# Optimization experiments

Measured on AMD Instinct MI355X. Metric: run time of the kernel, lower is better.

Reference implementation:

```python
import jax, jax.numpy as jnp
import numpy as np

B, S, D, H, F = 64, 256, 512, 8, 2048
NB = 2
L = NB + 2 * NB  # blocks_1 (NB) + blocks_2 (2*NB) = 6 attention layers
DH = D // H
FC1, FC2 = 512, 256  # final_fc_dim, final_fc_dim // 2


def setup_inputs() -> dict:
    key = jax.random.key(0)
    ks = jax.random.split(key, 32)
    w = lambda k, shape, s: jax.random.normal(k, shape, dtype=jnp.float32) * s
    sD = D ** -0.5
    return {
        "q_embed_data": w(ks[0], (B, S, D), 1.0),
        "qa_embed_data": w(ks[1], (B, S, D), 1.0),
        "Wq": w(ks[2], (L, D, D), sD), "bq": jnp.zeros((L, D), jnp.float32),
        "Wk": w(ks[3], (L, D, D), sD), "bk": jnp.zeros((L, D), jnp.float32),
        "Wv": w(ks[4], (L, D, D), sD), "bv": jnp.zeros((L, D), jnp.float32),
        "Wo": w(ks[5], (L, D, D), sD), "bo": jnp.zeros((L, D), jnp.float32),
        "gammas": w(ks[6], (L, H), 1.0),
        "ln1_g": jnp.ones((L, D), jnp.float32), "ln1_b": jnp.zeros((L, D), jnp.float32),
        "W1": w(ks[7], (L, D, F), sD), "b1": jnp.zeros((L, F), jnp.float32),
        "W2": w(ks[8], (L, F, D), F ** -0.5), "b2": jnp.zeros((L, D), jnp.float32),
        "ln2_g": jnp.ones((L, D), jnp.float32), "ln2_b": jnp.zeros((L, D), jnp.float32),
        "O1": w(ks[9], (2 * D, FC1), (2 * D) ** -0.5), "bO1": jnp.zeros((FC1,), jnp.float32),
        "O2": w(ks[10], (FC1, FC2), FC1 ** -0.5), "bO2": jnp.zeros((FC2,), jnp.float32),
        "O3": w(ks[11], (FC2, 1), FC2 ** -0.5), "bO3": jnp.zeros((1,), jnp.float32),
    }


def _layer_norm(x, g, b):
    mu = x.mean(-1, keepdims=True)
    var = ((x - mu) ** 2).mean(-1, keepdims=True)
    return (x - mu) * jax.lax.rsqrt(var + 1e-5) * g + b


def _akt_attention(q, k, v, mask, gamma, zero_pad):
    # q,k,v: [B,H,S,DH]; mask: [S,S] bool; gamma: [H]
    neg = jnp.float32(-1e32)
    scores = jnp.einsum('bhqd,bhkd->bhqk', q, k) / np.sqrt(DH).astype(np.float32)
    # monotonic distance-decay (detached in the original): softmax'd scores -> cumulative distance
    sm = jax.nn.softmax(jnp.where(mask, scores, neg), axis=-1) * mask
    sm = jax.lax.stop_gradient(sm)
    distcum = jnp.cumsum(sm, axis=-1)
    disttot = jnp.sum(sm, axis=-1, keepdims=True)
    idx = jnp.arange(S)
    pos = jnp.abs(idx[:, None] - idx[None, :]).astype(jnp.float32)  # |x1 - x2|
    dist = jnp.sqrt(jnp.clip((disttot - distcum) * pos, 0.0, None))
    g = -jax.nn.softplus(gamma)[None, :, None, None]
    total_effect = jnp.clip(jnp.exp(dist * g), 1e-5, 1e5)
    scores = jnp.where(mask, scores * total_effect, neg)
    attn = jax.nn.softmax(scores, axis=-1)
    if zero_pad:
        attn = attn.at[:, :, 0, :].set(0.0)  # zero first query row
    out = jnp.einsum('bhqk,bhkd->bhqd', attn, v)
    return out, attn


def reference(q_embed_data, qa_embed_data, Wq, bq, Wk, bk, Wv, bv, Wo, bo, gammas,
              ln1_g, ln1_b, W1, b1, W2, b2, ln2_g, ln2_b, O1, bO1, O2, bO2, O3, bO3):
    idx = jnp.arange(S)
    mask_incl = idx[:, None] >= idx[None, :]  # mask==1: current + past
    mask_excl = idx[:, None] > idx[None, :]   # mask==0: strictly past

    def block(i, query, key_, vals, incl, zero_pad, apply_pos):
        proj = lambda x, W, b: (x @ W + b).reshape(B, S, H, DH).transpose(0, 2, 1, 3)
        qh, kh, vh = proj(query, Wq[i], bq[i]), proj(key_, Wk[i], bk[i]), proj(vals, Wv[i], bv[i])
        o, attn = _akt_attention(qh, kh, vh, mask_incl if incl else mask_excl, gammas[i], zero_pad)
        o = o.transpose(0, 2, 1, 3).reshape(B, S, D) @ Wo[i] + bo[i]
        q2 = _layer_norm(query + o, ln1_g[i], ln1_b[i])
        if apply_pos:
            h = jax.nn.relu(q2 @ W1[i] + b1[i]) @ W2[i] + b2[i]
            q2 = _layer_norm(q2 + h, ln2_g[i], ln2_b[i])
        return q2, attn

    y = qa_embed_data
    x = q_embed_data
    li = 0
    for _ in range(NB):  # blocks_1: knowledge encoder, self-attn, mask=1
        y, _ = block(li, y, y, y, incl=True, zero_pad=False, apply_pos=True)
        li += 1
    attn = None
    flag_first = True
    for _ in range(2 * NB):  # blocks_2: alternating question self-attn / knowledge retriever
        if flag_first:
            x, _ = block(li, x, x, x, incl=True, zero_pad=False, apply_pos=False)
            flag_first = False
        else:
            x, attn = block(li, x, x, y, incl=False, zero_pad=True, apply_pos=True)
            flag_first = True
        li += 1

    concat_q = jnp.concatenate([x, q_embed_data], axis=-1)  # [B,S,2D]
    h = jax.nn.relu(concat_q @ O1 + bO1)
    h = jax.nn.relu(h @ O2 + bO2)
    preds = jax.nn.sigmoid((h @ O3 + bO3)[..., 0])  # [B,S]
    return preds
```

## Files before the change

kernel.cpp:

```cpp
#include <hip/hip_runtime.h>

typedef unsigned short u16;
typedef unsigned int u32;
typedef short short8 __attribute__((ext_vector_type(8)));
typedef float f32x4 __attribute__((ext_vector_type(4)));

#define DEV static __device__ __forceinline__

DEV u16 f2bf(float f) {
  u32 u = __builtin_bit_cast(u32, f);
  u32 r = u + 0x7FFFu + ((u >> 16) & 1u);
  return (u16)(r >> 16);
}
DEV float bf2f(u16 h) { u32 u = ((u32)h) << 16; return __builtin_bit_cast(float, u); }

DEV u32 cvtpk(float lo, float hi_) {
  u32 r;
  asm("v_cvt_pk_bf16_f32 %0, %1, %2" : "=v"(r) : "v"(lo), "v"(hi_));
  return r;
}

DEV void async16(const u16* g, u16* l) {
  __builtin_amdgcn_global_load_lds((const __attribute__((address_space(1))) void*)g,
                                   (__attribute__((address_space(3))) void*)l, 16, 0, 0);
}

template<bool RELU, bool OUTBF, bool RESID, bool SPLIT3>
__global__ __launch_bounds__(256, 2) void gemm_kernel(
    const u16* __restrict__ A, const u16* __restrict__ A2, int KA,
    int lda, int lda2,
    const u16* __restrict__ Bt, int K,
    const float* __restrict__ bias, const float* __restrict__ resid,
    float* __restrict__ Cf, u16* __restrict__ Cb, u16* __restrict__ Cb2, u16* __restrict__ Cb3,
    int ldc)
{
  __shared__ u16 smem[2][16384];
  const int tid = threadIdx.x, wave = tid >> 6, lane = tid & 63;
  const int m0 = blockIdx.x * 128, n0 = blockIdx.y * 128;
  const int wr = wave >> 1, wc = wave & 1;
  const int lj = lane & 15, hi = lane >> 4;

  f32x4 acc[4][4];
  const f32x4 zz = {0.f, 0.f, 0.f, 0.f};
#pragma unroll
  for (int i = 0; i < 4; i++)
#pragma unroll
    for (int j = 0; j < 4; j++) acc[i][j] = zz;

  const int nkt = K / 64;

  auto stage = [&](int buf, int kt) {
    int kofs = kt * 64;
    const u16* sa; int la;
    if (kofs < KA) { sa = A + kofs; la = lda; }
    else           { sa = A2 + (kofs - KA); la = lda2; }
#pragma unroll
    for (int i = 0; i < 8; i++) {
      int c = wave * 8 + i;
      if (c < 16) {
        const u16* g = sa + (size_t)(m0 + c * 8 + (lane >> 3)) * la + (lane & 7) * 8;
        async16(g, &smem[buf][c * 512]);
      } else {
        const u16* g = Bt + (size_t)(n0 + (c - 16) * 8 + (lane >> 3)) * K + kofs + (lane & 7) * 8;
        async16(g, &smem[buf][c * 512]);
      }
    }
  };

  stage(0, 0);
  int cur = 0;
  for (int kt = 0; kt < nkt; kt++) {
    __syncthreads();
    if (kt + 1 < nkt) stage(cur ^ 1, kt + 1);
    const u16* la_ = &smem[cur][0];
    const u16* lb_ = &smem[cur][8192];
#pragma unroll
    for (int ks = 0; ks < 2; ks++) {
      short8 af[4], bfr[4];
#pragma unroll
      for (int mi = 0; mi < 4; mi++)
        af[mi] = *(const short8*)(la_ + (wr * 64 + mi * 16 + lj) * 64 + ks * 32 + hi * 8);
#pragma unroll
      for (int ni = 0; ni < 4; ni++)
        bfr[ni] = *(const short8*)(lb_ + (wc * 64 + ni * 16 + lj) * 64 + ks * 32 + hi * 8);
#pragma unroll
      for (int mi = 0; mi < 4; mi++)
#pragma unroll
        for (int ni = 0; ni < 4; ni++)
          acc[mi][ni] = __builtin_amdgcn_mfma_f32_16x16x32_bf16(af[mi], bfr[ni], acc[mi][ni], 0, 0, 0);
    }
    cur ^= 1;
  }

  u16* outB = Cb;
  int nloc = n0;
  if (SPLIT3) {
    int sec = n0 >> 9;
    outB = (sec == 0) ? Cb : (sec == 1) ? Cb2 : Cb3;
    nloc = n0 & 511;
  }

  float bv[4];
#pragma unroll
  for (int ni = 0; ni < 4; ni++) bv[ni] = bias[n0 + wc * 64 + ni * 16 + lj];
#pragma unroll
  for (int mi = 0; mi < 4; mi++)
#pragma unroll
    for (int r = 0; r < 4; r++) {
      int row = m0 + wr * 64 + mi * 16 + hi * 4 + r;
      size_t rb = (size_t)row * ldc;
#pragma unroll
      for (int ni = 0; ni < 4; ni++) {
        int col = nloc + wc * 64 + ni * 16 + lj;
        float v = acc[mi][ni][r] + bv[ni];
        if (RESID) v += resid[rb + col];
        if (RELU) v = fmaxf(v, 0.f);
        if (OUTBF) outB[rb + col] = f2bf(v);
        else Cf[rb + col] = v;
      }
    }
}

template<bool RELU, bool SPLIT3>
__global__ __launch_bounds__(512) void gemm256_kernel(
    const u16* __restrict__ A, int lda,
    const u16* __restrict__ Bt, int K,
    const float* __restrict__ bias,
    u16* __restrict__ Cb, u16* __restrict__ Cb2, u16* __restrict__ Cb3, int ldc)
{
  __shared__ u16 smem[65536];
  const int tid = threadIdx.x, wave = tid >> 6, lane = tid & 63;
  const int m0 = blockIdx.x * 256, n0 = blockIdx.y * 256;
  const int wm = wave >> 2, wn = wave & 3;
  const int lj = lane & 15, hi = lane >> 4;
  const int srow = wave * 8 + (lane >> 3);
  const int schunk = (lane & 7) ^ ((lane >> 3) & 7);

  f32x4 acc[8][4];
  const f32x4 zz = {0.f, 0.f, 0.f, 0.f};
#pragma unroll
  for (int i = 0; i < 8; i++)
#pragma unroll
    for (int j = 0; j < 4; j++) acc[i][j] = zz;

  const int nkt = K / 64;

  auto stageA = [&](int buf, int kt, int seg) {
    const u16* g = A + (size_t)(m0 + seg * 64 + srow) * lda + kt * 64 + schunk * 8;
    async16(g, &smem[buf * 16384 + (seg * 64 + wave * 8) * 64]);
  };
  auto stageB = [&](int buf, int kt, int seg) {
    const u16* g = Bt + (size_t)(n0 + seg * 64 + srow) * K + kt * 64 + schunk * 8;
    async16(g, &smem[32768 + buf * 16384 + (seg * 64 + wave * 8) * 64]);
  };

#pragma unroll
  for (int seg = 0; seg < 4; seg++) stageA(0, 0, seg);
#pragma unroll
  for (int seg = 0; seg < 4; seg++) stageB(0, 0, seg);

  int cur = 0;
  for (int t = 0; t < nkt; t++) {
    const bool pf = (t + 1 < nkt);
    const char* aB = (const char*)smem + cur * 32768;
    const char* bB = (const char*)smem + 65536 + cur * 32768;
#pragma unroll
    for (int ph = 0; ph < 4; ph++) {
      const int mh = ph >> 1, nh = ph & 1;
      if (pf) {
        if (ph < 2) { stageA(cur ^ 1, t + 1, ph * 2); stageA(cur ^ 1, t + 1, ph * 2 + 1); }
        else        { stageB(cur ^ 1, t + 1, (ph - 2) * 2); stageB(cur ^ 1, t + 1, (ph - 2) * 2 + 1); }
      }
      if (ph == 0) {
        if (pf) asm volatile("s_waitcnt vmcnt(2)" ::: "memory");
        else    asm volatile("s_waitcnt vmcnt(0)" ::: "memory");
      }
      __builtin_amdgcn_s_barrier();

      short8 af[4][2], bfr[2][2];
#pragma unroll
      for (int mi = 0; mi < 4; mi++) {
        int row = wm * 128 + (mh * 4 + mi) * 16 + lj;
#pragma unroll
        for (int ks = 0; ks < 2; ks++)
          af[mi][ks] = *(const short8*)(aB + row * 128 + ((ks * 64 + hi * 16) ^ ((row & 7) << 4)));
      }
#pragma unroll
      for (int ni = 0; ni < 2; ni++) {
        int row = wn * 64 + (nh * 2 + ni) * 16 + lj;
#pragma unroll
        for (int ks = 0; ks < 2; ks++)
          bfr[ni][ks] = *(const short8*)(bB + row * 128 + ((ks * 64 + hi * 16) ^ ((row & 7) << 4)));
      }
      __builtin_amdgcn_s_setprio(1);
#pragma unroll
      for (int mi = 0; mi < 4; mi++)
#pragma unroll
        for (int ni = 0; ni < 2; ni++)
#pragma unroll
          for (int ks = 0; ks < 2; ks++)
            acc[mh * 4 + mi][nh * 2 + ni] =
                __builtin_amdgcn_mfma_f32_16x16x32_bf16(af[mi][ks], bfr[ni][ks],
                                                        acc[mh * 4 + mi][nh * 2 + ni], 0, 0, 0);
      __builtin_amdgcn_s_setprio(0);
      __builtin_amdgcn_s_barrier();
    }
    cur ^= 1;
  }

  u16* outB = Cb;
  int nloc = n0;
  if (SPLIT3) {
    int sec = n0 >> 9;
    outB = (sec == 0) ? Cb : (sec == 1) ? Cb2 : Cb3;
    nloc = n0 & 511;
  }

  float bv[4];
#pragma unroll
  for (int ni = 0; ni < 4; ni++) bv[ni] = bias[n0 + wn * 64 + ni * 16 + lj];
#pragma unroll
  for (int mi = 0; mi < 8; mi++)
#pragma unroll
    for (int r = 0; r < 4; r++) {
      int row = m0 + wm * 128 + mi * 16 + hi * 4 + r;
      size_t rb = (size_t)row * ldc;
#pragma unroll
      for (int ni = 0; ni < 4; ni++) {
        int col = nloc + wn * 64 + ni * 16 + lj;
        float v = acc[mi][ni][r] + bv[ni];
        if (RELU) v = fmaxf(v, 0.f);
        outB[rb + col] = f2bf(v);
      }
    }
}

__global__ __launch_bounds__(512) void gemmln_kernel(
    const u16* __restrict__ A, int lda,
    const u16* __restrict__ Bt, int K,
    const float* __restrict__ bias, const float* __restrict__ resid,
    const float* __restrict__ gamma, const float* __restrict__ beta,
    float* __restrict__ outF, u16* __restrict__ outB)
{
  __shared__ u16 smem[73728];
  const int tid = threadIdx.x, wave = tid >> 6, lane = tid & 63;
  const int m0 = blockIdx.x * 64;
  const int lj = lane & 15, hi = lane >> 4;
  const int srow = lane >> 3;
  const int schunk = (lane & 7) ^ ((lane >> 3) & 7);

  f32x4 acc[4][4];
  const f32x4 zz = {0.f, 0.f, 0.f, 0.f};
#pragma unroll
  for (int i = 0; i < 4; i++)
#pragma unroll
    for (int j = 0; j < 4; j++) acc[i][j] = zz;

  const int nkt = K / 64;

  auto stageA = [&](int buf, int kt) {
    const u16* g = A + (size_t)(m0 + wave * 8 + srow) * lda + kt * 64 + schunk * 8;
    async16(g, &smem[buf * 4096 + (wave * 8) * 64]);
  };
  auto stageB = [&](int buf, int kt, int seg) {
    const u16* g = Bt + (size_t)(seg * 64 + wave * 8 + srow) * K + kt * 64 + schunk * 8;
    async16(g, &smem[8192 + buf * 32768 + (seg * 64 + wave * 8) * 64]);
  };

  stageA(0, 0);
#pragma unroll
  for (int seg = 0; seg < 8; seg++) stageB(0, 0, seg);

  int cur = 0;
  for (int t = 0; t < nkt; t++) {
    const bool pf = (t + 1 < nkt);
    if (pf) {
      stageA(cur ^ 1, t + 1);
#pragma unroll
      for (int seg = 0; seg < 8; seg++) stageB(cur ^ 1, t + 1, seg);
    }
    if (pf) asm volatile("s_waitcnt vmcnt(9)" ::: "memory");
    else    asm volatile("s_waitcnt vmcnt(0)" ::: "memory");
    __builtin_amdgcn_s_barrier();

    const char* aB = (const char*)smem + cur * 8192;
    const char* bB = (const char*)smem + 16384 + cur * 65536;
    short8 af[4][2], bfr[4][2];
#pragma unroll
    for (int mi = 0; mi < 4; mi++) {
      int row = mi * 16 + lj;
#pragma unroll
      for (int ks = 0; ks < 2; ks++)
        af[mi][ks] = *(const short8*)(aB + row * 128 + ((ks * 64 + hi * 16) ^ ((row & 7) << 4)));
    }
#pragma unroll
    for (int ni = 0; ni < 4; ni++) {
      int row = wave * 64 + ni * 16 + lj;
#pragma unroll
      for (int ks = 0; ks < 2; ks++)
        bfr[ni][ks] = *(const short8*)(bB + row * 128 + ((ks * 64 + hi * 16) ^ ((row & 7) << 4)));
    }
    __builtin_amdgcn_s_setprio(1);
#pragma unroll
    for (int mi = 0; mi < 4; mi++)
#pragma unroll
      for (int ni = 0; ni < 4; ni++)
#pragma unroll
        for (int ks = 0; ks < 2; ks++)
          acc[mi][ni] = __builtin_amdgcn_mfma_f32_16x16x32_bf16(af[mi][ks], bfr[ni][ks],
                                                                acc[mi][ni], 0, 0, 0);
    __builtin_amdgcn_s_setprio(0);
    __builtin_amdgcn_s_barrier();
    cur ^= 1;
  }

  float bv[4], gv[4], btv[4];
  int col[4];
#pragma unroll
  for (int ni = 0; ni < 4; ni++) {
    col[ni] = wave * 64 + ni * 16 + lj;
    bv[ni] = bias[col[ni]];
    gv[ni] = gamma[col[ni]];
    btv[ni] = beta[col[ni]];
  }

  float* red = (float*)smem;

#pragma unroll
  for (int mi = 0; mi < 4; mi++)
#pragma unroll
    for (int r = 0; r < 4; r++) {
      int lrow = mi * 16 + hi * 4 + r;
      size_t rb = (size_t)(m0 + lrow) * 512;
      float s = 0.f, q = 0.f;
#pragma unroll
      for (int ni = 0; ni < 4; ni++) {
        float v = acc[mi][ni][r] + bv[ni] + resid[rb + col[ni]];
        acc[mi][ni][r] = v;
        s += v; q += v * v;
      }
#pragma unroll
      for (int m = 1; m <= 8; m <<= 1) { s += __shfl_xor(s, m); q += __shfl_xor(q, m); }
      if (lj == 0) { red[lrow * 16 + wave * 2] = s; red[lrow * 16 + wave * 2 + 1] = q; }
    }
  __syncthreads();

#pragma unroll
  for (int mi = 0; mi < 4; mi++)
#pragma unroll
    for (int r = 0; r < 4; r++) {
      int lrow = mi * 16 + hi * 4 + r;
      size_t rb = (size_t)(m0 + lrow) * 512;
      float s = 0.f, q = 0.f;
#pragma unroll
      for (int w = 0; w < 8; w++) { s += red[lrow * 16 + w * 2]; q += red[lrow * 16 + w * 2 + 1]; }
      float mu = s * (1.f / 512.f);
      float var = q * (1.f / 512.f) - mu * mu;
      float rs = rsqrtf(fmaxf(var, 0.f) + 1e-5f);
#pragma unroll
      for (int ni = 0; ni < 4; ni++) {
        float y = (acc[mi][ni][r] - mu) * rs * gv[ni] + btv[ni];
        outF[rb + col[ni]] = y;
        outB[rb + col[ni]] = f2bf(y);
      }
    }
}

template<bool INCL, bool ZP>
__global__ __launch_bounds__(512) void attn_kernel(
    const u16* __restrict__ qb, const u16* __restrict__ kb, const u16* __restrict__ vb,
    u16* __restrict__ ob, const float* __restrict__ gammas, int li)
{
  __shared__ u16 smem[32768];
  const int tid = threadIdx.x, wave = tid >> 6, lane = tid & 63;
  const int h = blockIdx.x, b = blockIdx.y;
  const int lj = lane & 15, hi = lane >> 4;
  const size_t rowbase = (size_t)b * 256 * 512 + h * 64;

#pragma unroll
  for (int p = 0; p < 2; p++) {
    int r2 = p * 128 + (tid >> 3) * 2;
    int cc = (tid & 7) * 8;
    union { uint4 v; u16 e[8]; } v0, v1;
    uint4 k0 = *(const uint4*)(kb + rowbase + (size_t)r2 * 512 + cc);
    uint4 k1 = *(const uint4*)(kb + rowbase + (size_t)(r2 + 1) * 512 + cc);
    v0.v = *(const uint4*)(vb + rowbase + (size_t)r2 * 512 + cc);
    v1.v = *(const uint4*)(vb + rowbase + (size_t)(r2 + 1) * 512 + cc);
    *(uint4*)((char*)smem + r2 * 128 + ((cc * 2) ^ ((r2 & 7) << 4))) = k0;
    *(uint4*)((char*)smem + (r2 + 1) * 128 + ((cc * 2) ^ (((r2 + 1) & 7) << 4))) = k1;
#pragma unroll
    for (int i = 0; i < 8; i++) {
      int d = cc + i;
      u32 pk = (u32)v0.e[i] | ((u32)v1.e[i] << 16);
      *(u32*)((char*)smem + 32768 + d * 512 + ((2 * r2) ^ ((d & 7) << 4))) = pk;
    }
  }

  const int qt0 = wave, qt1 = 15 - wave;

  short8 qfa[2][2];
#pragma unroll
  for (int cf = 0; cf < 2; cf++) {
    int t = cf ? qt1 : qt0;
#pragma unroll
    for (int s = 0; s < 2; s++)
      qfa[cf][s] = *(const short8*)(qb + rowbase + (size_t)(t * 16 + lj) * 512 + s * 32 + hi * 8);
  }

  float gm = gammas[li * 8 + h];
  float geff = -(gm > 20.f ? gm : log1pf(__expf(gm)));

  __syncthreads();

  const f32x4 zz = {0.f, 0.f, 0.f, 0.f};
  const int hsel = hi >> 1;
  const int sbase = lj + 32 * (hi & 1);

#pragma unroll
  for (int cf = 0; cf < 2; cf++) {
    const int t = cf ? qt1 : qt0;
    const int qb0 = t * 16;
    const int q = qb0 + lj;
    const int nrf = t + 1;
    const int nsp = (t + 2) >> 1;

    f32x4 acc[16], E[16];
#pragma unroll
    for (int rf = 0; rf < 16; rf++) acc[rf] = zz;

#pragma unroll
    for (int rf = 0; rf < 16; rf++) {
      if (rf >= nrf) continue;
      int row = rf * 16 + lj;
#pragma unroll
      for (int s = 0; s < 2; s++) {
        short8 kf = *(const short8*)((char*)smem + row * 128 + ((s * 64 + hi * 16) ^ ((row & 7) << 4)));
        acc[rf] = __builtin_amdgcn_mfma_f32_16x16x32_bf16(kf, qfa[cf][s], acc[rf], 0, 0, 0);
      }
    }

    float mx = -1e30f;
#pragma unroll
    for (int rf = 0; rf < 16; rf++) {
      if (rf >= nrf) continue;
#pragma unroll
      for (int r = 0; r < 4; r++) {
        acc[rf][r] *= 0.125f;
        int k = rf * 16 + hi * 4 + r;
        bool valid = INCL ? (k <= q) : (k < q);
        mx = fmaxf(mx, valid ? acc[rf][r] : -1e30f);
      }
    }
    mx = fmaxf(mx, __shfl_xor(mx, 16));
    mx = fmaxf(mx, __shfl_xor(mx, 32));
    float sum = 0.f;
#pragma unroll
    for (int rf = 0; rf < 16; rf++) {
      if (rf >= nrf) continue;
#pragma unroll
      for (int r = 0; r < 4; r++) {
        int k = rf * 16 + hi * 4 + r;
        bool valid = INCL ? (k <= q) : (k < q);
        float ev = valid ? __expf(acc[rf][r] - mx) : 0.f;
        E[rf][r] = ev;
        sum += ev;
      }
    }
    sum += __shfl_xor(sum, 16);
    sum += __shfl_xor(sum, 32);
    float inv1 = sum > 0.f ? 1.f / sum : 0.f;
    float dtot = sum > 0.f ? 1.f : 0.f;

    float run = 0.f;
#pragma unroll
    for (int rf = 0; rf < 16; rf++) {
      if (rf >= nrf) continue;
      float p[4];
      float pa = 0.f;
#pragma unroll
      for (int r = 0; r < 4; r++) {
        pa += E[rf][r] * inv1;
        p[r] = pa;
      }
      float tl = p[3];
      float v = tl;
      float u1 = __shfl_up(v, 16); v += (hi >= 1) ? u1 : 0.f;
      float u2 = __shfl_up(v, 32); v += (hi >= 2) ? u2 : 0.f;
      float T = __shfl(v, lj + 48);
      float cbase = run + (v - tl);
#pragma unroll
      for (int r = 0; r < 4; r++) {
        int k = rf * 16 + hi * 4 + r;
        bool valid = INCL ? (k <= q) : (k < q);
        float tail = fmaxf(dtot - (cbase + p[r]), 0.f);
        float pos = (float)(q - k);
        float dist = sqrtf(tail * pos);
        float te = fmaxf(__expf(dist * geff), 1e-5f);
        acc[rf][r] = valid ? acc[rf][r] * te : -1e32f;
      }
      run += T;
    }

    float mx2 = -3.0e38f;
#pragma unroll
    for (int rf = 0; rf < 16; rf++) {
      if (rf >= nrf) continue;
#pragma unroll
      for (int r = 0; r < 4; r++) mx2 = fmaxf(mx2, acc[rf][r]);
    }
    mx2 = fmaxf(mx2, __shfl_xor(mx2, 16));
    mx2 = fmaxf(mx2, __shfl_xor(mx2, 32));
    float sum2 = 0.f;
#pragma unroll
    for (int rf = 0; rf < 16; rf++) {
      if (rf >= nrf) continue;
#pragma unroll
      for (int r = 0; r < 4; r++) {
        float ev = __expf(acc[rf][r] - mx2);
        acc[rf][r] = ev;
        sum2 += ev;
      }
    }
    sum2 += __shfl_xor(sum2, 16);
    sum2 += __shfl_xor(sum2, 32);
    float inv = 1.f / sum2;
    if (ZP) { if (q == 0) inv = 0.f; }
#pragma unroll
    for (int rf = 0; rf < 16; rf++) {
      if (rf >= nrf) continue;
#pragma unroll
      for (int r = 0; r < 4; r++) acc[rf][r] *= inv;
    }

    f32x4 oacc[4];
#pragma unroll
    for (int j = 0; j < 4; j++) oacc[j] = zz;

#pragma unroll
    for (int sp = 0; sp < 8; sp++) {
      if (sp >= nsp) continue;
      u32 a0 = cvtpk(acc[2 * sp][0],     acc[2 * sp][1]);
      u32 a1 = cvtpk(acc[2 * sp][2],     acc[2 * sp][3]);
      u32 b0 = cvtpk(acc[2 * sp + 1][0], acc[2 * sp + 1][1]);
      u32 b1 = cvtpk(acc[2 * sp + 1][2], acc[2 * sp + 1][3]);
      u32 pw[4];
#pragma unroll
      for (int tt = 0; tt < 4; tt++) {
        int src = sbase + 16 * (tt >> 1);
        u32 za = (u32)__shfl((int)((tt & 1) ? a1 : a0), src);
        u32 zb = (u32)__shfl((int)((tt & 1) ? b1 : b0), src);
        pw[tt] = hsel ? zb : za;
      }
      short8 pf = __builtin_bit_cast(short8, *(uint4*)pw);
#pragma unroll
      for (int nf = 0; nf < 4; nf++) {
        int d = nf * 16 + lj;
        short8 vf = *(const short8*)((char*)smem + 32768 + d * 512 + ((sp * 64 + hi * 16) ^ ((d & 7) << 4)));
        oacc[nf] = __builtin_amdgcn_mfma_f32_16x16x32_bf16(pf, vf, oacc[nf], 0, 0, 0);
      }
    }

#pragma unroll
    for (int r = 0; r < 4; r++) {
      int qr = qb0 + hi * 4 + r;
      size_t obase = (size_t)(b * 256 + qr) * 512 + h * 64;
#pragma unroll
      for (int nf = 0; nf < 4; nf++)
        ob[obase + nf * 16 + lj] = f2bf(oacc[nf][r]);
    }
  }
}

__global__ void cvt_kernel(const float* __restrict__ in, u16* __restrict__ out, int n8)
{
  int i = blockIdx.x * 256 + threadIdx.x;
  if (i >= n8) return;
  float4 a = ((const float4*)in)[2 * i], c = ((const float4*)in)[2 * i + 1];
  union { uint4 v; u16 e[8]; } pk;
  pk.e[0]=f2bf(a.x); pk.e[1]=f2bf(a.y); pk.e[2]=f2bf(a.z); pk.e[3]=f2bf(a.w);
  pk.e[4]=f2bf(c.x); pk.e[5]=f2bf(c.y); pk.e[6]=f2bf(c.z); pk.e[7]=f2bf(c.w);
  ((uint4*)out)[i] = pk.v;
}

__global__ void trans_kernel(const float* __restrict__ in, u16* __restrict__ out,
                             int R, int C, size_t istr, size_t ostr)
{
  __shared__ float tile[32][33];
  in += (size_t)blockIdx.z * istr;
  out += (size_t)blockIdx.z * ostr;
  int c0 = blockIdx.x * 32, r0 = blockIdx.y * 32;
  int tx = threadIdx.x & 31, ty = threadIdx.x >> 5;
#pragma unroll
  for (int i = 0; i < 4; i++) tile[ty + i * 8][tx] = in[(size_t)(r0 + ty + i * 8) * C + c0 + tx];
  __syncthreads();
#pragma unroll
  for (int i = 0; i < 4; i++) out[(size_t)(c0 + ty + i * 8) * R + r0 + tx] = f2bf(tile[tx][ty + i * 8]);
}

__global__ void bias_concat_kernel(const float* __restrict__ bq, const float* __restrict__ bk,
                                   const float* __restrict__ bv, float* __restrict__ out)
{
  int t = blockIdx.x * 256 + threadIdx.x;
  if (t >= 6 * 1536) return;
  int li = t / 1536, c = t % 1536;
  float v = (c < 512) ? bq[li * 512 + c]
          : (c < 1024) ? bk[li * 512 + c - 512]
                       : bv[li * 512 + c - 1024];
  out[t] = v;
}

__global__ __launch_bounds__(256) void pred_kernel(const u16* __restrict__ h2,
    const float* __restrict__ O3, const float* __restrict__ bO3, float* __restrict__ out)
{
  int row = blockIdx.x * 4 + (threadIdx.x >> 6), lane = threadIdx.x & 63;
  union { uint2 v; u16 e[4]; } hv;
  hv.v = *(const uint2*)(h2 + (size_t)row * 256 + lane * 4);
  float d = 0.f;
#pragma unroll
  for (int i = 0; i < 4; i++) d += bf2f(hv.e[i]) * O3[lane * 4 + i];
#pragma unroll
  for (int m = 1; m <= 32; m <<= 1) d += __shfl_xor(d, m);
  if (lane == 0) out[row] = 1.f / (1.f + expf(-(d + bO3[0])));
}

extern "C" void kernel_launch(void* const* d_in, const int* in_sizes, int n_in,
                              void* d_out, int out_size, void* d_ws, size_t ws_size,
                              hipStream_t stream)
{
  const float* qe   = (const float*)d_in[0];
  const float* qa   = (const float*)d_in[1];
  const float* Wq   = (const float*)d_in[2];  const float* bq  = (const float*)d_in[3];
  const float* Wk   = (const float*)d_in[4];  const float* bk  = (const float*)d_in[5];
  const float* Wv   = (const float*)d_in[6];  const float* bv  = (const float*)d_in[7];
  const float* Wo   = (const float*)d_in[8];  const float* bo  = (const float*)d_in[9];
  const float* gam  = (const float*)d_in[10];
  const float* ln1g = (const float*)d_in[11]; const float* ln1b = (const float*)d_in[12];
  const float* W1   = (const float*)d_in[13]; const float* b1  = (const float*)d_in[14];
  const float* W2   = (const float*)d_in[15]; const float* b2  = (const float*)d_in[16];
  const float* ln2g = (const float*)d_in[17]; const float* ln2b = (const float*)d_in[18];
  const float* O1   = (const float*)d_in[19]; const float* bO1 = (const float*)d_in[20];
  const float* O2   = (const float*)d_in[21]; const float* bO2 = (const float*)d_in[22];
  const float* O3   = (const float*)d_in[23]; const float* bO3 = (const float*)d_in[24];
  float* preds = (float*)d_out;

  const int M = 16384;
  const int BIG = 0x3fffffff;
  char* ws = (char*)d_ws;
  size_t off = 0;
  auto alloc = [&](size_t bytes) { char* p = ws + off; off += (bytes + 255) & ~(size_t)255; return p; };

  u16* wqkvt = (u16*)alloc((size_t)6*1536*512*2);
  u16* wot   = (u16*)alloc((size_t)6*512*512*2);
  u16* w1t   = (u16*)alloc((size_t)6*2048*512*2);
  u16* w2t   = (u16*)alloc((size_t)6*512*2048*2);
  u16* o1t   = (u16*)alloc((size_t)512*1024*2);
  u16* o2t   = (u16*)alloc((size_t)256*512*2);
  float* bqkv = (float*)alloc((size_t)6*1536*4);
  u16* qx  = (u16*)alloc((size_t)M*512*2);
  u16* sA  = (u16*)alloc((size_t)M*512*2);
  u16* sB  = (u16*)alloc((size_t)M*512*2);
  float* g1 = (float*)alloc((size_t)M*512*4);
  u16* region = (u16*)alloc((size_t)M*2048*2);
  u16* qbf = region;
  u16* kbf = region + (size_t)M*512;
  u16* vbf = region + (size_t)2*M*512;
  u16* obf = region + (size_t)3*M*512;
  u16* h1  = region;
  u16* hd1 = region;
  u16* hd2 = region + (size_t)2*M*512;
  (void)ws_size; (void)in_sizes; (void)n_in; (void)out_size;

  trans_kernel<<<dim3(16, 16, 6), 256, 0, stream>>>(Wq, wqkvt,                          512, 512,  (size_t)512*512,  (size_t)1536*512);
  trans_kernel<<<dim3(16, 16, 6), 256, 0, stream>>>(Wk, wqkvt + (size_t)512*512,        512, 512,  (size_t)512*512,  (size_t)1536*512);
  trans_kernel<<<dim3(16, 16, 6), 256, 0, stream>>>(Wv, wqkvt + (size_t)1024*512,       512, 512,  (size_t)512*512,  (size_t)1536*512);
  trans_kernel<<<dim3(16, 16, 6), 256, 0, stream>>>(Wo, wot,                            512, 512,  (size_t)512*512,  (size_t)512*512);
  trans_kernel<<<dim3(64, 16, 6), 256, 0, stream>>>(W1, w1t,                            512, 2048, (size_t)512*2048, (size_t)2048*512);
  trans_kernel<<<dim3(16, 64, 6), 256, 0, stream>>>(W2, w2t,                            2048, 512, (size_t)2048*512, (size_t)512*2048);
  trans_kernel<<<dim3(16, 32, 1), 256, 0, stream>>>(O1, o1t,                            1024, 512, 0, 0);
  trans_kernel<<<dim3(8, 16, 1),  256, 0, stream>>>(O2, o2t,                            512, 256,  0, 0);
  bias_concat_kernel<<<36, 256, 0, stream>>>(bq, bk, bv, bqkv);
  cvt_kernel<<<4096, 256, 0, stream>>>(qe, qx, M * 512 / 8);
  cvt_kernel<<<4096, 256, 0, stream>>>(qa, sA, M * 512 / 8);

  const u16* curB = sA;
  const float* curF = qa;
  const u16* yfin = nullptr;
  const dim3 gA(8, 64);

  for (int li = 0; li < 6; li++) {
    bool ffn  = (li == 0 || li == 1 || li == 3 || li == 5);
    bool excl = (li == 3 || li == 5);
    size_t wqkv_off = (size_t)li * 1536 * 512;

    if (!excl) {
      gemm256_kernel<false, true><<<dim3(64, 6), 512, 0, stream>>>(
          curB, 512, wqkvt + wqkv_off, 512, bqkv + li * 1536, qbf, kbf, vbf, 512);
    } else {
      gemm256_kernel<false, true><<<dim3(64, 4), 512, 0, stream>>>(
          curB, 512, wqkvt + wqkv_off, 512, bqkv + li * 1536, qbf, kbf, nullptr, 512);
      gemm_kernel<false, true, false, false><<<dim3(128, 4), 256, 0, stream>>>(
          yfin, yfin, BIG, 512, 512, wqkvt + wqkv_off + (size_t)1024 * 512, 512, bv + li * 512,
          nullptr, nullptr, vbf, nullptr, nullptr, 512);
    }

    if (!excl) attn_kernel<true,  false><<<gA, 512, 0, stream>>>(qbf, kbf, vbf, obf, gam, li);
    else       attn_kernel<false, true ><<<gA, 512, 0, stream>>>(qbf, kbf, vbf, obf, gam, li);

    gemmln_kernel<<<256, 512, 0, stream>>>(
        obf, 512, wot + (size_t)li * 512 * 512, 512, bo + li * 512,
        curF, ln1g + li * 512, ln1b + li * 512, g1, sB);
    curB = sB; curF = g1;

    if (ffn) {
      gemm256_kernel<true, false><<<dim3(64, 8), 512, 0, stream>>>(
          curB, 512, w1t + (size_t)li * 2048 * 512, 512, b1 + li * 2048, h1, nullptr, nullptr, 2048);
      u16* nB = (li < 2) ? sA : sB;
      gemmln_kernel<<<256, 512, 0, stream>>>(
          h1, 2048, w2t + (size_t)li * 512 * 2048, 2048, b2 + li * 512,
          g1, ln2g + li * 512, ln2b + li * 512, g1, nB);
      curB = nB;
    }
    if (li == 1) { yfin = curB; curB = qx; curF = qe; }
  }

  gemm_kernel<true, true, false, false><<<dim3(128, 4), 256, 0, stream>>>(
      curB, qx, 512, 512, 512, o1t, 1024, bO1, nullptr, nullptr, hd1, nullptr, nullptr, 512);
  gemm_kernel<true, true, false, false><<<dim3(128, 2), 256, 0, stream>>>(
      hd1, hd1, BIG, 512, 512, o2t, 512, bO2, nullptr, nullptr, hd2, nullptr, nullptr, 256);
  pred_kernel<<<4096, 256, 0, stream>>>(hd2, O3, bO3, preds);
}
```

Before: 1.282 ms.

## Fuse exclusive-layer V projection into QKV GEMM and pack two heads per attention block

The QKV GEMM now takes a second A source, which the third N-segment (the V columns) reads from. This lets the cross-attention layers compute V from the encoder output inside the same launch instead of issuing a separate smaller GEMM. The attention kernel now runs 1024 threads per block, each covering two heads with 64KB of LDS per head. This halves the grid and makes blocks larger. The fusion saves a launch and uses the GPU better, while the larger blocks may cut occupancy because the LDS use doubles.

```diff
diff --git a/kernel.cpp b/kernel.cpp
--- a/kernel.cpp
+++ b/kernel.cpp
@@ -123,7 +123,7 @@
 
 template<bool RELU, bool SPLIT3>
 __global__ __launch_bounds__(512) void gemm256_kernel(
-    const u16* __restrict__ A, int lda,
+    const u16* __restrict__ A, const u16* __restrict__ A2v, int lda,
     const u16* __restrict__ Bt, int K,
     const float* __restrict__ bias,
     u16* __restrict__ Cb, u16* __restrict__ Cb2, u16* __restrict__ Cb3, int ldc)
@@ -136,6 +136,8 @@
   const int srow = wave * 8 + (lane >> 3);
   const int schunk = (lane & 7) ^ ((lane >> 3) & 7);
 
+  const u16* Asrc = (SPLIT3 && (n0 >> 9) == 2 && A2v) ? A2v : A;
+
   f32x4 acc[8][4];
   const f32x4 zz = {0.f, 0.f, 0.f, 0.f};
 #pragma unroll
@@ -146,7 +148,7 @@
   const int nkt = K / 64;
 
   auto stageA = [&](int buf, int kt, int seg) {
-    const u16* g = A + (size_t)(m0 + seg * 64 + srow) * lda + kt * 64 + schunk * 8;
+    const u16* g = Asrc + (size_t)(m0 + seg * 64 + srow) * lda + kt * 64 + schunk * 8;
     async16(g, &smem[buf * 16384 + (seg * 64 + wave * 8) * 64]);
   };
   auto stageB = [&](int buf, int kt, int seg) {
@@ -367,36 +369,39 @@
 }
 
 template<bool INCL, bool ZP>
-__global__ __launch_bounds__(512) void attn_kernel(
+__global__ __launch_bounds__(1024) void attn_kernel(
     const u16* __restrict__ qb, const u16* __restrict__ kb, const u16* __restrict__ vb,
     u16* __restrict__ ob, const float* __restrict__ gammas, int li)
 {
-  __shared__ u16 smem[32768];
+  __shared__ u16 smem[65536];
   const int tid = threadIdx.x, wave = tid >> 6, lane = tid & 63;
-  const int h = blockIdx.x, b = blockIdx.y;
+  const int hloc = wave >> 3, wv = wave & 7;
+  const int h = blockIdx.x * 2 + hloc, b = blockIdx.y;
   const int lj = lane & 15, hi = lane >> 4;
   const size_t rowbase = (size_t)b * 256 * 512 + h * 64;
-
+  char* sb = (char*)smem + hloc * 65536;
+
+  const int tloc = tid & 511;
 #pragma unroll
   for (int p = 0; p < 2; p++) {
-    int r2 = p * 128 + (tid >> 3) * 2;
-    int cc = (tid & 7) * 8;
+    int r2 = p * 128 + (tloc >> 3) * 2;
+    int cc = (tloc & 7) * 8;
     union { uint4 v; u16 e[8]; } v0, v1;
     uint4 k0 = *(const uint4*)(kb + rowbase + (size_t)r2 * 512 + cc);
     uint4 k1 = *(const uint4*)(kb + rowbase + (size_t)(r2 + 1) * 512 + cc);
     v0.v = *(const uint4*)(vb + rowbase + (size_t)r2 * 512 + cc);
     v1.v = *(const uint4*)(vb + rowbase + (size_t)(r2 + 1) * 512 + cc);
-    *(uint4*)((char*)smem + r2 * 128 + ((cc * 2) ^ ((r2 & 7) << 4))) = k0;
-    *(uint4*)((char*)smem + (r2 + 1) * 128 + ((cc * 2) ^ (((r2 + 1) & 7) << 4))) = k1;
+    *(uint4*)(sb + r2 * 128 + ((cc * 2) ^ ((r2 & 7) << 4))) = k0;
+    *(uint4*)(sb + (r2 + 1) * 128 + ((cc * 2) ^ (((r2 + 1) & 7) << 4))) = k1;
 #pragma unroll
     for (int i = 0; i < 8; i++) {
       int d = cc + i;
       u32 pk = (u32)v0.e[i] | ((u32)v1.e[i] << 16);
-      *(u32*)((char*)smem + 32768 + d * 512 + ((2 * r2) ^ ((d & 7) << 4))) = pk;
-    }
-  }
-
-  const int qt0 = wave, qt1 = 15 - wave;
+      *(u32*)(sb + 32768 + d * 512 + ((2 * r2) ^ ((d & 7) << 4))) = pk;
+    }
+  }
+
+  const int qt0 = wv, qt1 = 15 - wv;
 
   short8 qfa[2][2];
 #pragma unroll
@@ -434,7 +439,7 @@
       int row = rf * 16 + lj;
 #pragma unroll
       for (int s = 0; s < 2; s++) {
-        short8 kf = *(const short8*)((char*)smem + row * 128 + ((s * 64 + hi * 16) ^ ((row & 7) << 4)));
+        short8 kf = *(const short8*)(sb + row * 128 + ((s * 64 + hi * 16) ^ ((row & 7) << 4)));
         acc[rf] = __builtin_amdgcn_mfma_f32_16x16x32_bf16(kf, qfa[cf][s], acc[rf], 0, 0, 0);
       }
     }
@@ -555,7 +560,7 @@
 #pragma unroll
       for (int nf = 0; nf < 4; nf++) {
         int d = nf * 16 + lj;
-        short8 vf = *(const short8*)((char*)smem + 32768 + d * 512 + ((sp * 64 + hi * 16) ^ ((d & 7) << 4)));
+        short8 vf = *(const short8*)(sb + 32768 + d * 512 + ((sp * 64 + hi * 16) ^ ((d & 7) << 4)));
         oacc[nf] = __builtin_amdgcn_mfma_f32_16x16x32_bf16(pf, vf, oacc[nf], 0, 0, 0);
       }
     }
@@ -685,26 +690,19 @@
   const u16* curB = sA;
   const float* curF = qa;
   const u16* yfin = nullptr;
-  const dim3 gA(8, 64);
+  const dim3 gA(4, 64);
 
   for (int li = 0; li < 6; li++) {
     bool ffn  = (li == 0 || li == 1 || li == 3 || li == 5);
     bool excl = (li == 3 || li == 5);
     size_t wqkv_off = (size_t)li * 1536 * 512;
 
-    if (!excl) {
-      gemm256_kernel<false, true><<<dim3(64, 6), 512, 0, stream>>>(
-          curB, 512, wqkvt + wqkv_off, 512, bqkv + li * 1536, qbf, kbf, vbf, 512);
-    } else {
-      gemm256_kernel<false, true><<<dim3(64, 4), 512, 0, stream>>>(
-          curB, 512, wqkvt + wqkv_off, 512, bqkv + li * 1536, qbf, kbf, nullptr, 512);
-      gemm_kernel<false, true, false, false><<<dim3(128, 4), 256, 0, stream>>>(
-          yfin, yfin, BIG, 512, 512, wqkvt + wqkv_off + (size_t)1024 * 512, 512, bv + li * 512,
-          nullptr, nullptr, vbf, nullptr, nullptr, 512);
-    }
-
-    if (!excl) attn_kernel<true,  false><<<gA, 512, 0, stream>>>(qbf, kbf, vbf, obf, gam, li);
-    else       attn_kernel<false, true ><<<gA, 512, 0, stream>>>(qbf, kbf, vbf, obf, gam, li);
+    gemm256_kernel<false, true><<<dim3(64, 6), 512, 0, stream>>>(
+        curB, excl ? yfin : curB, 512, wqkvt + wqkv_off, 512, bqkv + li * 1536,
+        qbf, kbf, vbf, 512);
+
+    if (!excl) attn_kernel<true,  false><<<gA, 1024, 0, stream>>>(qbf, kbf, vbf, obf, gam, li);
+    else       attn_kernel<false, true ><<<gA, 1024, 0, stream>>>(qbf, kbf, vbf, obf, gam, li);
 
     gemmln_kernel<<<256, 512, 0, stream>>>(
         obf, 512, wot + (size_t)li * 512 * 512, 512, bo + li * 512,
@@ -713,7 +711,8 @@
 
     if (ffn) {
       gemm256_kernel<true, false><<<dim3(64, 8), 512, 0, stream>>>(
-          curB, 512, w1t + (size_t)li * 2048 * 512, 512, b1 + li * 2048, h1, nullptr, nullptr, 2048);
+          curB, nullptr, 512, w1t + (size_t)li * 2048 * 512, 512, b1 + li * 2048,
+          h1, nullptr, nullptr, 2048);
       u16* nB = (li < 2) ? sA : sB;
       gemmln_kernel<<<256, 512, 0, stream>>>(
           h1, 2048, w2t + (size_t)li * 512 * 2048, 2048, b2 + li * 512,
```

Result: slower. 1.447 ms (+12.9%).
